# Kernel optimization log

Measured on AMD Instinct MI355X. Metric: run time of the kernel, lower is better.

## Reference

```python
import jax, jax.numpy as jnp
import numpy as np

B, C, Hd, Wd = 8, 256, 64, 64
NUM_HEAD = 4
RATIO = 0.25
OUT_CH = int(NUM_HEAD * C * RATIO)      # 256
HEAD_DIM = OUT_CH // NUM_HEAD           # 64
EPS = 1e-5


def conv1x1(x, w, b=None):
    # x: [B,Ci,H,W], w: [Co,Ci]
    y = jnp.einsum('bchw,oc->bohw', x, w)
    if b is not None:
        y = y + b[None, :, None, None]
    return y


def setup_inputs() -> dict:
    key = jax.random.key(0)
    ks = jax.random.split(key, 16)
    s = lambda fan: 1.0 / np.sqrt(fan)
    return {
        'key':   jax.random.normal(ks[0], (B, C, Hd, Wd), jnp.float32),
        'query': jax.random.normal(ks[1], (B, C, Hd, Wd), jnp.float32),
        'wq': jax.random.normal(ks[2], (OUT_CH, C), jnp.float32) * s(C),
        'bq': jax.random.normal(ks[3], (OUT_CH,), jnp.float32) * 0.01,
        'wk': jax.random.normal(ks[4], (OUT_CH, C), jnp.float32) * s(C),
        'bk': jax.random.normal(ks[5], (OUT_CH,), jnp.float32) * 0.01,
        'wv': jax.random.normal(ks[6], (OUT_CH, C), jnp.float32) * s(C),
        'bv': jax.random.normal(ks[7], (OUT_CH,), jnp.float32) * 0.01,
        'wW': jax.random.normal(ks[8], (C, HEAD_DIM), jnp.float32) * s(HEAD_DIM),
        'bn_gamma': jnp.ones((C,), jnp.float32),
        'bn_beta': jnp.zeros((C,), jnp.float32),
        'bn_mean': jax.random.normal(ks[9], (C,), jnp.float32) * 0.1,
        'bn_var': jax.random.uniform(ks[10], (C,), jnp.float32, 0.5, 1.5),
        'w3': jax.random.normal(ks[11], (C, 2 * C, 3, 3), jnp.float32) * s(2 * C * 9),
        'b3': jax.random.normal(ks[12], (C,), jnp.float32) * 0.01,
        'w1': jax.random.normal(ks[13], (C, C), jnp.float32) * s(C),
        'b1': jax.random.normal(ks[14], (C,), jnp.float32) * 0.01,
    }


def reference(key, query, wq, bq, wk, bk, wv, bv, wW,
              bn_gamma, bn_beta, bn_mean, bn_var, w3, b3, w1, b1):
    b, c, h, w = query.shape
    q = conv1x1(query, wq, bq).reshape(b, NUM_HEAD, HEAD_DIM, h, w)
    k = conv1x1(key, wk, bk).reshape(b, NUM_HEAD, HEAD_DIM, h, w)
    v = conv1x1(key, wv, bv).reshape(b, NUM_HEAD, HEAD_DIM, h, w)

    att = (q * k).sum(axis=2) / np.sqrt(OUT_CH)          # [b, num_head, h, w]
    sm = jax.nn.softmax(att, axis=1)[:, :, None]         # softmax over heads
    weighted = (v * sm).sum(axis=1)                      # [b, head_dim, h, w]

    # W: 1x1 conv (no bias) + BatchNorm (inference)
    out = conv1x1(weighted, wW)
    inv = bn_gamma / jnp.sqrt(bn_var + EPS)
    out = out * inv[None, :, None, None] + (bn_beta - bn_mean * inv)[None, :, None, None]

    # fuse: ConvBlock (reflect-pad 3x3 conv + ELU) then 1x1 conv
    x = jnp.concatenate([key, out], axis=1)              # [b, 2C, h, w]
    x = jnp.pad(x, ((0, 0), (0, 0), (1, 1), (1, 1)), mode='reflect')
    x = jax.lax.conv_general_dilated(x, w3, (1, 1), 'VALID',
                                     dimension_numbers=('NCHW', 'OIHW', 'NCHW'))
    x = jax.nn.elu(x + b3[None, :, None, None])
    return conv1x1(x, w1, b1)
```

## Files before the change

### kernel.cpp

```cpp
#include <hip/hip_runtime.h>
#include <hip/hip_bf16.h>

typedef unsigned short u16;
typedef unsigned int u32;
typedef short bf16x8 __attribute__((ext_vector_type(8)));
typedef float f32x4 __attribute__((ext_vector_type(4)));

#define NPX 32768

__device__ __forceinline__ u16 f2bf(float f) {
  union { float f; u32 u; } v; v.f = f;
  return (u16)((v.u + 0x7FFFu + ((v.u >> 16) & 1u)) >> 16);
}

__device__ __forceinline__ void gload16(const u16* g, u16* l) {
  __builtin_amdgcn_global_load_lds(
      (const __attribute__((address_space(1))) void*)g,
      (__attribute__((address_space(3))) void*)l, 16, 0, 0);
}


__global__ __launch_bounds__(256) void prep_small(
    const float* __restrict__ wq, const float* __restrict__ wk,
    const float* __restrict__ wv, const float* __restrict__ w1,
    const float* __restrict__ wW, const float* __restrict__ gamma,
    const float* __restrict__ beta, const float* __restrict__ mean,
    const float* __restrict__ var,
    u16* __restrict__ wqb, u16* __restrict__ wkb, u16* __restrict__ wvb,
    u16* __restrict__ w1b, u16* __restrict__ wWpb, float* __restrict__ bWp) {
  int idx = blockIdx.x * 256 + threadIdx.x;
  if (idx < 65536) {
    int o = idx >> 8, c = idx & 255;
    int dst = (c >> 5) * 8192 + o * 32 + ((c >> 3) & 3) * 8 + (c & 7);
    wqb[dst] = f2bf(wq[idx]);
    wkb[dst] = f2bf(wk[idx]);
    wvb[dst] = f2bf(wv[idx]);
    w1b[dst] = f2bf(w1[idx]);
  } else if (idx < 65536 + 16384) {
    int j = idx - 65536;
    int o = j >> 6, c = j & 63;
    float inv = gamma[o] * rsqrtf(var[o] + 1e-5f);
    int dst = (c >> 5) * 8192 + o * 32 + ((c >> 3) & 3) * 8 + (c & 7);
    wWpb[dst] = f2bf(wW[j] * inv);
  } else if (idx < 65536 + 16384 + 256) {
    int o = idx - 65536 - 16384;
    float inv = gamma[o] * rsqrtf(var[o] + 1e-5f);
    bWp[o] = beta[o] - mean[o] * inv;
  }
}

__global__ __launch_bounds__(256) void prep_w3t(const float* __restrict__ w3,
                                                u16* __restrict__ w3c) {
  int idx = blockIdx.x * 256 + threadIdx.x;
  int o = idx >> 9, c = idx & 511;
  int cb = c >> 5;
  int lk = (c >> 3) & 3, e = c & 7;
  #pragma unroll
  for (int t = 0; t < 9; ++t)
    w3c[(size_t)(cb * 9 + t) * 8192 + o * 32 + lk * 8 + e] =
        f2bf(w3[idx * 9 + t]);
}

__global__ __launch_bounds__(256, 2) void attn_kernel(
    const float* __restrict__ qsrc, const float* __restrict__ ksrc,
    u16* __restrict__ xcat,
    const u16* __restrict__ wqb, const u16* __restrict__ wkb, const u16* __restrict__ wvb,
    const float* __restrict__ bq, const float* __restrict__ bk, const float* __restrict__ bv,
    const u16* __restrict__ wWpb, const float* __restrict__ bWp) {
  __shared__ __align__(16) char smem[74752];
  u16* aq = (u16*)smem;
  u16* ak = (u16*)(smem + 32768);
  u16* tile = (u16*)(smem + 65536);
  float* att_s = (float*)(smem + 65536);
  u16* wsum = (u16*)(smem + 66560);
  float* wbuf = (float*)smem;
  u16* ob = (u16*)smem;

  int tid = threadIdx.x;
  int lane = tid & 63, wv_ = tid >> 6;
  int lc = lane & 15, lk = lane >> 4;
  int px0 = blockIdx.x * 64;
  int b = px0 >> 12, hw0 = px0 & 4095;

  #pragma unroll
  for (int t = 0; t < 8; ++t) {
    const float* src = (t < 4) ? qsrc : ksrc;
    int cc = t & 3;
    #pragma unroll
    for (int i = 0; i < 4; ++i) {
      int idx = tid + 256 * i;
      int c = idx >> 4, p4 = idx & 15;
      const float4 v = *(const float4*)&src[(size_t)(b * 256 + cc * 64 + c) * 4096 + hw0 + p4 * 4];
      u32 lo = f2bf(v.x) | ((u32)f2bf(v.y) << 16);
      u32 hi = f2bf(v.z) | ((u32)f2bf(v.w) << 16);
      *(uint2*)&tile[c * 72 + p4 * 4] = make_uint2(lo, hi);
    }
    __syncthreads();
    int px = tid >> 2, cq = tid & 3;
    u32 vv[8];
    #pragma unroll
    for (int i = 0; i < 8; ++i) {
      u16 a = tile[(cq * 16 + 2 * i) * 72 + px];
      u16 bb = tile[(cq * 16 + 2 * i + 1) * 72 + px];
      vv[i] = a | ((u32)bb << 16);
    }
    u16* dstl = (t < 4) ? aq : ak;
    int c8 = cc * 8 + cq * 2;
    *(uint4*)(dstl + px * 256 + (c8 ^ (px & 7)) * 8) = make_uint4(vv[0], vv[1], vv[2], vv[3]);
    *(uint4*)(dstl + px * 256 + ((c8 + 1) ^ (px & 7)) * 8) = make_uint4(vv[4], vv[5], vv[6], vv[7]);
    if (t >= 4) {
      u16* dp = xcat + (size_t)(px0 + px) * 512 + cc * 64 + cq * 16;
      *(uint4*)dp = make_uint4(vv[0], vv[1], vv[2], vv[3]);
      *(uint4*)(dp + 8) = make_uint4(vv[4], vv[5], vv[6], vv[7]);
    }
    __syncthreads();
  }

  f32x4 zero4 = {0.f, 0.f, 0.f, 0.f};
  f32x4 accq[4][4], acck[4][4];
  #pragma unroll
  for (int mi = 0; mi < 4; ++mi)
    #pragma unroll
    for (int nj = 0; nj < 4; ++nj) { accq[mi][nj] = zero4; acck[mi][nj] = zero4; }

  #pragma unroll
  for (int kk = 0; kk < 8; ++kk) {
    bf16x8 afq[4], afk[4], bfq[4], bfk[4];
    #pragma unroll
    for (int mi = 0; mi < 4; ++mi) {
      int px = mi * 16 + lc;
      int s = (kk * 4 + lk) ^ (px & 7);
      afq[mi] = *(const bf16x8*)(aq + px * 256 + s * 8);
      afk[mi] = *(const bf16x8*)(ak + px * 256 + s * 8);
    }
    #pragma unroll
    for (int nj = 0; nj < 4; ++nj) {
      int n = wv_ * 64 + nj * 16 + lc;
      bfq[nj] = *(const bf16x8*)(wqb + kk * 8192 + n * 32 + lk * 8);
      bfk[nj] = *(const bf16x8*)(wkb + kk * 8192 + n * 32 + lk * 8);
    }
    #pragma unroll
    for (int mi = 0; mi < 4; ++mi)
      #pragma unroll
      for (int nj = 0; nj < 4; ++nj) {
        accq[mi][nj] = __builtin_amdgcn_mfma_f32_16x16x32_bf16(afq[mi], bfq[nj], accq[mi][nj], 0, 0, 0);
        acck[mi][nj] = __builtin_amdgcn_mfma_f32_16x16x32_bf16(afk[mi], bfk[nj], acck[mi][nj], 0, 0, 0);
      }
  }

  #pragma unroll
  for (int nj = 0; nj < 4; ++nj) {
    float bqv = bq[wv_ * 64 + nj * 16 + lc];
    float bkv = bk[wv_ * 64 + nj * 16 + lc];
    #pragma unroll
    for (int mi = 0; mi < 4; ++mi)
      #pragma unroll
      for (int j = 0; j < 4; ++j) { accq[mi][nj][j] += bqv; acck[mi][nj][j] += bkv; }
  }

  float smx[4][4];
  #pragma unroll
  for (int mi = 0; mi < 4; ++mi)
    #pragma unroll
    for (int j = 0; j < 4; ++j) {
      float p = 0.f;
      #pragma unroll
      for (int nj = 0; nj < 4; ++nj) p += accq[mi][nj][j] * acck[mi][nj][j];
      p += __shfl_xor(p, 1);
      p += __shfl_xor(p, 2);
      p += __shfl_xor(p, 4);
      p += __shfl_xor(p, 8);
      float a = p * 0.0625f;
      smx[mi][j] = a;
      if (lc == 0) att_s[wv_ * 64 + mi * 16 + lk * 4 + j] = a;
    }
  __syncthreads();
  #pragma unroll
  for (int mi = 0; mi < 4; ++mi)
    #pragma unroll
    for (int j = 0; j < 4; ++j) {
      int px = mi * 16 + lk * 4 + j;
      float a0 = att_s[px], a1 = att_s[64 + px], a2 = att_s[128 + px], a3 = att_s[192 + px];
      float mx = fmaxf(fmaxf(a0, a1), fmaxf(a2, a3));
      float e0 = __expf(a0 - mx), e1 = __expf(a1 - mx);
      float e2 = __expf(a2 - mx), e3 = __expf(a3 - mx);
      float den = e0 + e1 + e2 + e3;
      float ew = wv_ == 0 ? e0 : (wv_ == 1 ? e1 : (wv_ == 2 ? e2 : e3));
      smx[mi][j] = ew / den;
    }

  f32x4 accv[4][4];
  #pragma unroll
  for (int mi = 0; mi < 4; ++mi)
    #pragma unroll
    for (int nj = 0; nj < 4; ++nj) accv[mi][nj] = zero4;
  #pragma unroll
  for (int kk = 0; kk < 8; ++kk) {
    bf16x8 af[4], bfr[4];
    #pragma unroll
    for (int mi = 0; mi < 4; ++mi) {
      int px = mi * 16 + lc;
      int s = (kk * 4 + lk) ^ (px & 7);
      af[mi] = *(const bf16x8*)(ak + px * 256 + s * 8);
    }
    #pragma unroll
    for (int nj = 0; nj < 4; ++nj) {
      int n = wv_ * 64 + nj * 16 + lc;
      bfr[nj] = *(const bf16x8*)(wvb + kk * 8192 + n * 32 + lk * 8);
    }
    #pragma unroll
    for (int mi = 0; mi < 4; ++mi)
      #pragma unroll
      for (int nj = 0; nj < 4; ++nj)
        accv[mi][nj] = __builtin_amdgcn_mfma_f32_16x16x32_bf16(af[mi], bfr[nj], accv[mi][nj], 0, 0, 0);
  }
  #pragma unroll
  for (int nj = 0; nj < 4; ++nj) {
    float bvv = bv[wv_ * 64 + nj * 16 + lc];
    #pragma unroll
    for (int mi = 0; mi < 4; ++mi)
      #pragma unroll
      for (int j = 0; j < 4; ++j) accv[mi][nj][j] += bvv;
  }
  __syncthreads();

  #pragma unroll
  for (int mi = 0; mi < 4; ++mi)
    #pragma unroll
    for (int nj = 0; nj < 4; ++nj)
      #pragma unroll
      for (int j = 0; j < 4; ++j) {
        int px = mi * 16 + lk * 4 + j;
        wbuf[(wv_ * 64 + px) * 64 + nj * 16 + lc] = smx[mi][j] * accv[mi][nj][j];
      }
  __syncthreads();

  #pragma unroll
  for (int i = 0; i < 2; ++i) {
    int idx = tid + 256 * i;
    int px = idx >> 3, c = idx & 7;
    float a8[8] = {0.f, 0.f, 0.f, 0.f, 0.f, 0.f, 0.f, 0.f};
    #pragma unroll
    for (int h = 0; h < 4; ++h) {
      const float4* p = (const float4*)(wbuf + ((h * 64 + px) * 64 + c * 8));
      float4 u0 = p[0], u1 = p[1];
      a8[0] += u0.x; a8[1] += u0.y; a8[2] += u0.z; a8[3] += u0.w;
      a8[4] += u1.x; a8[5] += u1.y; a8[6] += u1.z; a8[7] += u1.w;
    }
    u32 p0 = f2bf(a8[0]) | ((u32)f2bf(a8[1]) << 16);
    u32 p1 = f2bf(a8[2]) | ((u32)f2bf(a8[3]) << 16);
    u32 p2 = f2bf(a8[4]) | ((u32)f2bf(a8[5]) << 16);
    u32 p3 = f2bf(a8[6]) | ((u32)f2bf(a8[7]) << 16);
    *(uint4*)(wsum + px * 64 + (c ^ (px & 7)) * 8) = make_uint4(p0, p1, p2, p3);
  }
  __syncthreads();

  f32x4 a4[4][4];
  #pragma unroll
  for (int mi = 0; mi < 4; ++mi)
    #pragma unroll
    for (int nj = 0; nj < 4; ++nj) a4[mi][nj] = zero4;
  #pragma unroll
  for (int kk = 0; kk < 2; ++kk) {
    bf16x8 af[4], bfr[4];
    #pragma unroll
    for (int mi = 0; mi < 4; ++mi) {
      int px = mi * 16 + lc;
      int s = (kk * 4 + lk) ^ (px & 7);
      af[mi] = *(const bf16x8*)(wsum + px * 64 + s * 8);
    }
    #pragma unroll
    for (int nj = 0; nj < 4; ++nj) {
      int n = wv_ * 64 + nj * 16 + lc;
      bfr[nj] = *(const bf16x8*)(wWpb + kk * 8192 + n * 32 + lk * 8);
    }
    #pragma unroll
    for (int mi = 0; mi < 4; ++mi)
      #pragma unroll
      for (int nj = 0; nj < 4; ++nj)
        a4[mi][nj] = __builtin_amdgcn_mfma_f32_16x16x32_bf16(af[mi], bfr[nj], a4[mi][nj], 0, 0, 0);
  }
  #pragma unroll
  for (int nj = 0; nj < 4; ++nj) {
    int o = wv_ * 64 + nj * 16 + lc;
    float bb = bWp[o];
    #pragma unroll
    for (int mi = 0; mi < 4; ++mi)
      #pragma unroll
      for (int j = 0; j < 4; ++j) {
        int px = mi * 16 + lk * 4 + j;
        ob[px * 264 + o] = f2bf(a4[mi][nj][j] + bb);
      }
  }
  __syncthreads();
  #pragma unroll
  for (int i = 0; i < 8; ++i) {
    int idx = tid + 256 * i;
    int px = idx >> 5, c8 = idx & 31;
    *(uint4*)(xcat + (size_t)(px0 + px) * 512 + 256 + c8 * 8) =
        *(const uint4*)(ob + px * 264 + c8 * 8);
  }
}

__global__ __launch_bounds__(512) void conv3_kernel(
    const u16* __restrict__ xcat, const u16* __restrict__ w3c,
    const float* __restrict__ b3, const u16* __restrict__ w1b,
    const float* __restrict__ b1, float* __restrict__ out) {
  __shared__ __align__(16) u16 smem[33792];
  u16* xb0 = smem;
  u16* xb1 = smem + 8704;

  int tid = threadIdx.x;
  int lane = tid & 63, wave = tid >> 6;
  int lc = lane & 15, lk = lane >> 4;
  int wr = wave >> 2, wc = wave & 3;
  int sbid = (blockIdx.x & 7) * 32 + (blockIdx.x >> 3);
  int b = sbid >> 5, r0 = (sbid & 31) * 2;

  int gx0, gx1, gx2;
  #pragma unroll
  for (int i = 0; i < 3; ++i) {
    int c = (i == 0) ? tid : (i == 1 ? tid + 512 : 1024 + lane);
    int q = c >> 2, slot = c & 3;
    int row = q / 68, px = q - row * 68;
    px = px < 66 ? px : 65;
    int h_in = r0 - 1 + row; h_in = h_in < 0 ? 1 : (h_in > 63 ? 62 : h_in);
    int w_in = px - 1;       w_in = w_in < 0 ? 1 : (w_in > 63 ? 62 : w_in);
    int g = ((b * 64 + h_in) * 64 + w_in) * 512 + slot * 8;
    if (i == 0) gx0 = g; else if (i == 1) gx1 = g; else gx2 = g;
  }
  int wo0 = ((wc * 64 + lc) * 4 + lk) * 8;

#define STAGE_X(dst, cb_)                                                       \
  do {                                                                          \
    asm volatile("" ::: "memory");                                              \
    gload16(xcat + gx0 + (cb_) * 32, (dst) + (size_t)tid * 8);                  \
    gload16(xcat + gx1 + (cb_) * 32, (dst) + (size_t)(tid + 512) * 8);          \
    gload16(xcat + gx2 + (cb_) * 32, (dst) + (size_t)(1024 + lane) * 8);        \
    asm volatile("" ::: "memory");                                              \
  } while (0)

#define PREF_W(SLOT, SLAB)                                                      \
  do {                                                                          \
    const u16* ws_ = w3c + (size_t)(SLAB) * 8192 + wo0;                         \
    Wr[SLOT][0] = *(const bf16x8*)(ws_);                                        \
    Wr[SLOT][1] = *(const bf16x8*)(ws_ + 512);                                  \
    Wr[SLOT][2] = *(const bf16x8*)(ws_ + 1024);                                 \
    Wr[SLOT][3] = *(const bf16x8*)(ws_ + 1536);                                 \
  } while (0)

  f32x4 zero4 = {0.f, 0.f, 0.f, 0.f};
  f32x4 acc[4][4];
  #pragma unroll
  for (int mi = 0; mi < 4; ++mi)
    #pragma unroll
    for (int nj = 0; nj < 4; ++nj) acc[mi][nj] = zero4;

  bf16x8 Wr[3][4];

  STAGE_X(xb0, 0);
  PREF_W(0, 0);
  PREF_W(1, 1);
  PREF_W(2, 2);
  asm volatile("s_waitcnt vmcnt(12)\n\ts_barrier" ::: "memory");

  for (int cb = 0; cb < 16; ++cb) {
    const u16* xcur = (cb & 1) ? xb1 : xb0;
    u16* xnxt = (cb & 1) ? xb0 : xb1;
#define TAP(T)                                                                  \
    {                                                                           \
      const int dy = (T) / 3, dx = (T) % 3;                                     \
      bf16x8 af[4];                                                             \
      _Pragma("unroll") for (int mi = 0; mi < 4; ++mi)                          \
        af[mi] = *(const bf16x8*)(xcur +                                        \
            (size_t)(((wr + dy) * 68 + mi * 16 + lc + dx) * 4 + lk) * 8);       \
      __builtin_amdgcn_s_setprio(1);                                            \
      _Pragma("unroll") for (int mi = 0; mi < 4; ++mi)                          \
        _Pragma("unroll") for (int nj = 0; nj < 4; ++nj)                        \
          acc[mi][nj] = __builtin_amdgcn_mfma_f32_16x16x32_bf16(                \
              af[mi], Wr[(T) % 3][nj], acc[mi][nj], 0, 0, 0);                   \
      __builtin_amdgcn_s_setprio(0);                                            \
      int slab_ = cb * 9 + (T) + 3;                                             \
      if (slab_ < 144) PREF_W((T) % 3, slab_);                                  \
      if ((T) == 5 && cb < 15) STAGE_X(xnxt, cb + 1);                           \
    }
    TAP(0) TAP(1) TAP(2) TAP(3) TAP(4) TAP(5) TAP(6) TAP(7) TAP(8)
#undef TAP
    if (cb < 15)
      asm volatile("s_waitcnt vmcnt(12)\n\ts_barrier" ::: "memory");
  }
#undef STAGE_X
#undef PREF_W

  __syncthreads();

  u16* eb = smem;
  #pragma unroll
  for (int nj = 0; nj < 4; ++nj) {
    int o = wc * 64 + nj * 16 + lc;
    float bias = b3[o];
    #pragma unroll
    for (int mi = 0; mi < 4; ++mi)
      #pragma unroll
      for (int j = 0; j < 4; ++j) {
        int p = wr * 64 + mi * 16 + lk * 4 + j;
        float v = acc[mi][nj][j] + bias;
        v = v > 0.f ? v : (__expf(v) - 1.f);
        eb[p * 264 + o] = f2bf(v);
      }
  }
  __syncthreads();

  f32x4 acc2[4][4];
  #pragma unroll
  for (int mi = 0; mi < 4; ++mi)
    #pragma unroll
    for (int nj = 0; nj < 4; ++nj) acc2[mi][nj] = zero4;
  #pragma unroll
  for (int kk = 0; kk < 8; ++kk) {
    bf16x8 af[4], bfr[4];
    #pragma unroll
    for (int mi = 0; mi < 4; ++mi)
      af[mi] = *(const bf16x8*)(eb + (size_t)(wr * 64 + mi * 16 + lc) * 264 + kk * 32 + lk * 8);
    #pragma unroll
    for (int nj = 0; nj < 4; ++nj)
      bfr[nj] = *(const bf16x8*)(w1b + kk * 8192 + (wc * 64 + nj * 16 + lc) * 32 + lk * 8);
    #pragma unroll
    for (int mi = 0; mi < 4; ++mi)
      #pragma unroll
      for (int nj = 0; nj < 4; ++nj)
        acc2[mi][nj] = __builtin_amdgcn_mfma_f32_16x16x32_bf16(af[mi], bfr[nj], acc2[mi][nj], 0, 0, 0);
  }
  #pragma unroll
  for (int nj = 0; nj < 4; ++nj) {
    int o = wc * 64 + nj * 16 + lc;
    float bias = b1[o];
    #pragma unroll
    for (int mi = 0; mi < 4; ++mi) {
      float4 v;
      v.x = acc2[mi][nj][0] + bias;
      v.y = acc2[mi][nj][1] + bias;
      v.z = acc2[mi][nj][2] + bias;
      v.w = acc2[mi][nj][3] + bias;
      *(float4*)&out[(size_t)(b * 256 + o) * 4096 + (r0 + wr) * 64 + mi * 16 + lk * 4] = v;
    }
  }
}

extern "C" void kernel_launch(void* const* d_in, const int* in_sizes, int n_in,
                              void* d_out, int out_size, void* d_ws, size_t ws_size,
                              hipStream_t stream) {
  const float* key   = (const float*)d_in[0];
  const float* query = (const float*)d_in[1];
  const float* wq    = (const float*)d_in[2];
  const float* bq    = (const float*)d_in[3];
  const float* wk    = (const float*)d_in[4];
  const float* bk    = (const float*)d_in[5];
  const float* wv    = (const float*)d_in[6];
  const float* bv    = (const float*)d_in[7];
  const float* wW    = (const float*)d_in[8];
  const float* gamma = (const float*)d_in[9];
  const float* beta  = (const float*)d_in[10];
  const float* mean  = (const float*)d_in[11];
  const float* var   = (const float*)d_in[12];
  const float* w3    = (const float*)d_in[13];
  const float* b3    = (const float*)d_in[14];
  const float* w1    = (const float*)d_in[15];
  const float* b1    = (const float*)d_in[16];
  float* out = (float*)d_out;

  char* ws = (char*)d_ws;
  u16* xcat  = (u16*)(ws + 16777216);
  u16* w3t   = (u16*)(ws + 67108864);
  u16* wqb   = (u16*)(ws + 69468160);
  u16* wkb   = (u16*)(ws + 69599232);
  u16* wvb   = (u16*)(ws + 69730304);
  u16* w1b   = (u16*)(ws + 69861376);
  u16* wWpb  = (u16*)(ws + 69992448);
  float* bWp = (float*)(ws + 70025216);

  prep_small<<<321, 256, 0, stream>>>(wq, wk, wv, w1, wW, gamma, beta, mean, var,
                                      wqb, wkb, wvb, w1b, wWpb, bWp);
  prep_w3t<<<512, 256, 0, stream>>>(w3, w3t);
  attn_kernel<<<512, 256, 0, stream>>>(query, key, xcat, wqb, wkb, wvb,
                                       bq, bk, bv, wWpb, bWp);
  conv3_kernel<<<256, 512, 0, stream>>>(xcat, w3t, b3, w1b, b1, out);
}
```

Measured before the change: 128.5 us.

## Swizzle conv3 LDS layout and restructure tap pipeline with explicit waits

The conv3 kernel now XOR-swizzles the 16-byte slot index when staging input tiles into LDS, so the per-tap fragment reads avoid bank conflicts. The tap loop is rewritten with alternating A-fragment registers, explicit lgkmcnt waits and sched barriers before each MFMA group, and a shifted weight-prefetch schedule that keeps two slabs in flight. The custom vmcnt barrier is replaced by __syncthreads, which may serialize global loads more than before. The LDS array grows slightly.

```diff
diff --git a/kernel.cpp b/kernel.cpp
--- a/kernel.cpp
+++ b/kernel.cpp
@@ -18,7 +18,6 @@
       (const __attribute__((address_space(1))) void*)g,
       (__attribute__((address_space(3))) void*)l, 16, 0, 0);
 }
-
 
 __global__ __launch_bounds__(256) void prep_small(
     const float* __restrict__ wq, const float* __restrict__ wk,
@@ -306,7 +305,7 @@
     const u16* __restrict__ xcat, const u16* __restrict__ w3c,
     const float* __restrict__ b3, const u16* __restrict__ w1b,
     const float* __restrict__ b1, float* __restrict__ out) {
-  __shared__ __align__(16) u16 smem[33792];
+  __shared__ __align__(16) u16 smem[34816];
   u16* xb0 = smem;
   u16* xb1 = smem + 8704;
 
@@ -320,8 +319,9 @@
   int gx0, gx1, gx2;
   #pragma unroll
   for (int i = 0; i < 3; ++i) {
-    int c = (i == 0) ? tid : (i == 1 ? tid + 512 : 1024 + lane);
-    int q = c >> 2, slot = c & 3;
+    int pc = (i == 0) ? tid : (i == 1 ? tid + 512 : 1024 + lane);
+    int q = pc >> 2;
+    int slot = (pc & 3) ^ ((q >> 1) & 3);
     int row = q / 68, px = q - row * 68;
     px = px < 66 ? px : 65;
     int h_in = r0 - 1 + row; h_in = h_in < 0 ? 1 : (h_in > 63 ? 62 : h_in);
@@ -333,20 +333,42 @@
 
 #define STAGE_X(dst, cb_)                                                       \
   do {                                                                          \
-    asm volatile("" ::: "memory");                                              \
     gload16(xcat + gx0 + (cb_) * 32, (dst) + (size_t)tid * 8);                  \
     gload16(xcat + gx1 + (cb_) * 32, (dst) + (size_t)(tid + 512) * 8);          \
     gload16(xcat + gx2 + (cb_) * 32, (dst) + (size_t)(1024 + lane) * 8);        \
-    asm volatile("" ::: "memory");                                              \
   } while (0)
 
 #define PREF_W(SLOT, SLAB)                                                      \
   do {                                                                          \
-    const u16* ws_ = w3c + (size_t)(SLAB) * 8192 + wo0;                         \
-    Wr[SLOT][0] = *(const bf16x8*)(ws_);                                        \
-    Wr[SLOT][1] = *(const bf16x8*)(ws_ + 512);                                  \
-    Wr[SLOT][2] = *(const bf16x8*)(ws_ + 1024);                                 \
-    Wr[SLOT][3] = *(const bf16x8*)(ws_ + 1536);                                 \
+    if ((SLAB) < 144) {                                                         \
+      const u16* ws_ = w3c + (size_t)(SLAB) * 8192 + wo0;                       \
+      Wr[SLOT][0] = *(const bf16x8*)(ws_);                                      \
+      Wr[SLOT][1] = *(const bf16x8*)(ws_ + 512);                                \
+      Wr[SLOT][2] = *(const bf16x8*)(ws_ + 1024);                               \
+      Wr[SLOT][3] = *(const bf16x8*)(ws_ + 1536);                               \
+    }                                                                           \
+  } while (0)
+
+#define ISSUE_AF(DST, TAP)                                                      \
+  do {                                                                          \
+    const int dy_ = (TAP) / 3, dx_ = (TAP) % 3;                                 \
+    _Pragma("unroll") for (int mi = 0; mi < 4; ++mi) {                          \
+      int q_ = (wr + dy_) * 68 + mi * 16 + lc + dx_;                            \
+      DST[mi] = *(const bf16x8*)(xcur +                                         \
+          (size_t)(q_ * 4 + (lk ^ ((q_ >> 1) & 3))) * 8);                       \
+    }                                                                           \
+  } while (0)
+
+#define MFMA_C(AFR, WS)                                                         \
+  do {                                                                          \
+    asm volatile("s_waitcnt lgkmcnt(0)" ::: "memory");                          \
+    __builtin_amdgcn_sched_barrier(0);                                          \
+    __builtin_amdgcn_s_setprio(1);                                              \
+    _Pragma("unroll") for (int mi = 0; mi < 4; ++mi)                            \
+      _Pragma("unroll") for (int nj = 0; nj < 4; ++nj)                          \
+        acc[mi][nj] = __builtin_amdgcn_mfma_f32_16x16x32_bf16(                  \
+            AFR[mi], Wr[WS][nj], acc[mi][nj], 0, 0, 0);                         \
+    __builtin_amdgcn_s_setprio(0);                                              \
   } while (0)
 
   f32x4 zero4 = {0.f, 0.f, 0.f, 0.f};
@@ -357,42 +379,51 @@
     for (int nj = 0; nj < 4; ++nj) acc[mi][nj] = zero4;
 
   bf16x8 Wr[3][4];
-
-  STAGE_X(xb0, 0);
+  bf16x8 afA[4], afB[4];
+
   PREF_W(0, 0);
   PREF_W(1, 1);
-  PREF_W(2, 2);
-  asm volatile("s_waitcnt vmcnt(12)\n\ts_barrier" ::: "memory");
+  STAGE_X(xb0, 0);
+  __syncthreads();
 
   for (int cb = 0; cb < 16; ++cb) {
     const u16* xcur = (cb & 1) ? xb1 : xb0;
     u16* xnxt = (cb & 1) ? xb0 : xb1;
-#define TAP(T)                                                                  \
-    {                                                                           \
-      const int dy = (T) / 3, dx = (T) % 3;                                     \
-      bf16x8 af[4];                                                             \
-      _Pragma("unroll") for (int mi = 0; mi < 4; ++mi)                          \
-        af[mi] = *(const bf16x8*)(xcur +                                        \
-            (size_t)(((wr + dy) * 68 + mi * 16 + lc + dx) * 4 + lk) * 8);       \
-      __builtin_amdgcn_s_setprio(1);                                            \
-      _Pragma("unroll") for (int mi = 0; mi < 4; ++mi)                          \
-        _Pragma("unroll") for (int nj = 0; nj < 4; ++nj)                        \
-          acc[mi][nj] = __builtin_amdgcn_mfma_f32_16x16x32_bf16(                \
-              af[mi], Wr[(T) % 3][nj], acc[mi][nj], 0, 0, 0);                   \
-      __builtin_amdgcn_s_setprio(0);                                            \
-      int slab_ = cb * 9 + (T) + 3;                                             \
-      if (slab_ < 144) PREF_W((T) % 3, slab_);                                  \
-      if ((T) == 5 && cb < 15) STAGE_X(xnxt, cb + 1);                           \
-    }
-    TAP(0) TAP(1) TAP(2) TAP(3) TAP(4) TAP(5) TAP(6) TAP(7) TAP(8)
-#undef TAP
-    if (cb < 15)
-      asm volatile("s_waitcnt vmcnt(12)\n\ts_barrier" ::: "memory");
-  }
+    int base = cb * 9;
+    ISSUE_AF(afA, 0);
+    MFMA_C(afA, 0);
+    PREF_W(2, base + 2);
+    ISSUE_AF(afB, 1);
+    MFMA_C(afB, 1);
+    PREF_W(0, base + 3);
+    ISSUE_AF(afA, 2);
+    MFMA_C(afA, 2);
+    PREF_W(1, base + 4);
+    ISSUE_AF(afB, 3);
+    MFMA_C(afB, 0);
+    PREF_W(2, base + 5);
+    ISSUE_AF(afA, 4);
+    MFMA_C(afA, 1);
+    PREF_W(0, base + 6);
+    if (cb < 15) STAGE_X(xnxt, cb + 1);
+    ISSUE_AF(afB, 5);
+    MFMA_C(afB, 2);
+    PREF_W(1, base + 7);
+    ISSUE_AF(afA, 6);
+    MFMA_C(afA, 0);
+    PREF_W(2, base + 8);
+    ISSUE_AF(afB, 7);
+    MFMA_C(afB, 1);
+    PREF_W(0, base + 9);
+    ISSUE_AF(afA, 8);
+    MFMA_C(afA, 2);
+    PREF_W(1, base + 10);
+    __syncthreads();
+  }
+#undef MFMA_C
+#undef ISSUE_AF
+#undef PREF_W
 #undef STAGE_X
-#undef PREF_W
-
-  __syncthreads();
 
   u16* eb = smem;
   #pragma unroll
```

After: 124.8 us. 1.03x faster.
